# Kernel tuning notes

Hardware: AMD Instinct MI355X
Metric: run time of the kernel (lower is better)

Reference implementation:

```python
import jax, jax.numpy as jnp
import numpy as np

RADIUS = 3
T_STEPS = 2
NEG = -9.0e8
B, L, DEG = 256, 64, 6
FEAT, BOND, FP, OUT = 39, 10, 256, 1


def _leaky(x):
    return jax.nn.leaky_relu(x, 0.01)


def _gru(x, h, wih, whh, bih, bhh):
    # PyTorch GRUCell: gates ordered (r, z, n)
    gi = x @ wih.T + bih
    gh = h @ whh.T + bhh
    ir, iz, inn = jnp.split(gi, 3, axis=-1)
    hr, hz, hn = jnp.split(gh, 3, axis=-1)
    r = jax.nn.sigmoid(ir + hr)
    z = jax.nn.sigmoid(iz + hz)
    n = jnp.tanh(inn + r * hn)
    return (1.0 - z) * n + z * h


def _forward(atom_list, bond_list, atom_mask,
             atom_fc_w, atom_fc_b, neighbor_fc_w, neighbor_fc_b,
             align_w, align_b, attend_w, attend_b,
             gru_wih, gru_whh, gru_bih, gru_bhh,
             mol_align_w, mol_align_b, mol_attend_w, mol_attend_b,
             mol_gru_wih, mol_gru_whh, mol_gru_bih, mol_gru_bhh,
             out_w, out_b,
             atom_degree_list, bond_degree_list):
    b, l, _ = atom_list.shape
    mask = atom_mask[..., None]                                   # [B,L,1]
    atom_feature = _leaky(atom_list @ atom_fc_w.T + atom_fc_b)    # [B,L,FP]

    # per-molecule neighbor gather (padding index = L-1)
    bidx = jnp.arange(b)[:, None, None]
    atom_nb = atom_list[bidx, atom_degree_list]                    # [B,L,deg,FEAT]
    bond_nb = bond_list[bidx, bond_degree_list]                    # [B,L,deg,BOND]
    neighbor_feature = _leaky(
        jnp.concatenate([atom_nb, bond_nb], axis=-1) @ neighbor_fc_w.T + neighbor_fc_b
    )                                                              # [B,L,deg,FP]

    attend_mask = (atom_degree_list != l - 1).astype(atom_feature.dtype)[..., None]
    softmax_mask = jnp.where(atom_degree_list == l - 1, NEG, 0.0).astype(atom_feature.dtype)[..., None]

    for d in range(RADIUS):
        af_exp = jnp.broadcast_to(atom_feature[:, :, None, :], neighbor_feature.shape)
        feature_align = jnp.concatenate([af_exp, neighbor_feature], axis=-1)  # [B,L,deg,2FP]
        align_score = _leaky(feature_align @ align_w[d].T + align_b[d]) + softmax_mask
        attention_weight = jax.nn.softmax(align_score, axis=-2) * attend_mask
        attended = neighbor_feature @ attend_w[d].T + attend_b[d]
        context = jax.nn.elu(jnp.sum(attention_weight * attended, axis=-2))   # [B,L,FP]
        atom_feature = _gru(context.reshape(b * l, -1), atom_feature.reshape(b * l, -1),
                            gru_wih[d], gru_whh[d], gru_bih[d], gru_bhh[d]).reshape(b, l, -1)
        # faithful to original: self-feature broadcast across neighbor dim
        neighbor_feature = jnp.broadcast_to(jax.nn.relu(atom_feature)[:, :, None, :],
                                            neighbor_feature.shape)

    mol_feature = jnp.sum(jax.nn.relu(atom_feature) * mask, axis=-2)          # [B,FP]
    mol_softmax_mask = jnp.where(atom_mask == 0, NEG, 0.0).astype(atom_feature.dtype)[..., None]

    for _ in range(T_STEPS):
        m_exp = jnp.broadcast_to(mol_feature[:, None, :], atom_feature.shape)
        mol_align = jnp.concatenate([m_exp, atom_feature], axis=-1)           # [B,L,2FP]
        mol_score = _leaky(mol_align @ mol_align_w.T + mol_align_b) + mol_softmax_mask
        mol_w = jax.nn.softmax(mol_score, axis=-2) * mask
        attended = atom_feature @ mol_attend_w.T + mol_attend_b
        mol_context = jax.nn.elu(jnp.sum(mol_w * attended, axis=-2))
        mol_feature = _gru(mol_context, mol_feature,
                           mol_gru_wih, mol_gru_whh, mol_gru_bih, mol_gru_bhh)

    mol_prediction = mol_feature @ out_w.T + out_b
    return atom_feature, mol_prediction


def setup_inputs() -> dict:
    key = jax.random.key(0)
    ks = jax.random.split(key, 20)
    s = 0.05
    return {
        "atom_list": jax.random.normal(ks[0], (B, L, FEAT), jnp.float32),
        "bond_list": jax.random.normal(ks[1], (B, L, BOND), jnp.float32),
        "atom_degree_list": jax.random.randint(ks[2], (B, L, DEG), 0, L),
        "bond_degree_list": jax.random.randint(ks[3], (B, L, DEG), 0, L),
        "atom_mask": jnp.ones((B, L), jnp.float32),
        "atom_fc_w": jax.random.normal(ks[4], (FP, FEAT)) * s,
        "atom_fc_b": jnp.zeros((FP,)),
        "neighbor_fc_w": jax.random.normal(ks[5], (FP, FEAT + BOND)) * s,
        "neighbor_fc_b": jnp.zeros((FP,)),
        "align_w": jax.random.normal(ks[6], (RADIUS, 1, 2 * FP)) * s,
        "align_b": jnp.zeros((RADIUS, 1)),
        "attend_w": jax.random.normal(ks[7], (RADIUS, FP, FP)) * s,
        "attend_b": jnp.zeros((RADIUS, FP)),
        "gru_wih": jax.random.normal(ks[8], (RADIUS, 3 * FP, FP)) * s,
        "gru_whh": jax.random.normal(ks[9], (RADIUS, 3 * FP, FP)) * s,
        "gru_bih": jnp.zeros((RADIUS, 3 * FP)),
        "gru_bhh": jnp.zeros((RADIUS, 3 * FP)),
        "mol_align_w": jax.random.normal(ks[10], (1, 2 * FP)) * s,
        "mol_align_b": jnp.zeros((1,)),
        "mol_attend_w": jax.random.normal(ks[11], (FP, FP)) * s,
        "mol_attend_b": jnp.zeros((FP,)),
        "mol_gru_wih": jax.random.normal(ks[12], (3 * FP, FP)) * s,
        "mol_gru_whh": jax.random.normal(ks[13], (3 * FP, FP)) * s,
        "mol_gru_bih": jnp.zeros((3 * FP,)),
        "mol_gru_bhh": jnp.zeros((3 * FP,)),
        "out_w": jax.random.normal(ks[14], (OUT, FP)) * s,
        "out_b": jnp.zeros((OUT,)),
    }


def reference(atom_list, bond_list, atom_degree_list, bond_degree_list, atom_mask,
              atom_fc_w, atom_fc_b, neighbor_fc_w, neighbor_fc_b,
              align_w, align_b, attend_w, attend_b,
              gru_wih, gru_whh, gru_bih, gru_bhh,
              mol_align_w, mol_align_b, mol_attend_w, mol_attend_b,
              mol_gru_wih, mol_gru_whh, mol_gru_bih, mol_gru_bhh,
              out_w, out_b):
    return _forward(atom_list, bond_list, atom_mask,
                    atom_fc_w, atom_fc_b, neighbor_fc_w, neighbor_fc_b,
                    align_w, align_b, attend_w, attend_b,
                    gru_wih, gru_whh, gru_bih, gru_bhh,
                    mol_align_w, mol_align_b, mol_attend_w, mol_attend_b,
                    mol_gru_wih, mol_gru_whh, mol_gru_bih, mol_gru_bhh,
                    out_w, out_b,
                    atom_degree_list, bond_degree_list)
```

## Files before the change

### kernel.cpp

```cpp
#include <hip/hip_runtime.h>
#include <hip/hip_bf16.h>

#define NB 256
#define NL 64
#define DEG 6
#define FEAT 39
#define BOND 10
#define FP 256
#define NEGV (-9.0e8f)

using s16x8 = __attribute__((ext_vector_type(8))) short;
using f32x4 = __attribute__((ext_vector_type(4))) float;

__device__ __forceinline__ unsigned short f2bf(float f){
  unsigned u = __float_as_uint(f);
  u += 0x7fffu + ((u >> 16) & 1u);
  return (unsigned short)(u >> 16);
}
__device__ __forceinline__ float lo16(unsigned u){ return __uint_as_float(u << 16); }
__device__ __forceinline__ float hi16(unsigned u){ return __uint_as_float(u & 0xffff0000u); }

__device__ __forceinline__ float block_sum256(float v, float* scr){
  #pragma unroll
  for(int o=32;o>0;o>>=1) v += __shfl_down(v, o, 64);
  __syncthreads();
  if((threadIdx.x & 63) == 0) scr[threadIdx.x >> 6] = v;
  __syncthreads();
  return scr[0] + scr[1] + scr[2] + scr[3];
}
__device__ __forceinline__ float wave_allsum(float v){
  #pragma unroll
  for(int o=1;o<64;o<<=1) v += __shfl_xor(v, o, 64);
  return v;
}

#define CVT_N0 196608
#define CVT_N1 589824
#define CVT_N2 589824
#define CVT_N3 65536
#define CVT_N4 196608
#define CVT_N5 196608
#define CVT_TOT (CVT_N0+CVT_N1+CVT_N2+CVT_N3+CVT_N4+CVT_N5)

__global__ void k_cvt_all(const float* __restrict__ a0, const float* __restrict__ a1,
                          const float* __restrict__ a2, const float* __restrict__ a3,
                          const float* __restrict__ a4, const float* __restrict__ a5,
                          unsigned short* __restrict__ dst){
  int i = blockIdx.x*256 + threadIdx.x;
  int off = i; const float* src;
  if(off < CVT_N0) src = a0;
  else { off -= CVT_N0;
    if(off < CVT_N1) src = a1;
    else { off -= CVT_N1;
      if(off < CVT_N2) src = a2;
      else { off -= CVT_N2;
        if(off < CVT_N3) src = a3;
        else { off -= CVT_N3;
          if(off < CVT_N4) src = a4;
          else { off -= CVT_N4; src = a5; } } } } }
  dst[i] = f2bf(src[off]);
}

__global__ void k_tr(const float* __restrict__ aw, const float* __restrict__ nw,
                     float* __restrict__ afcT, unsigned short* __restrict__ nfcT){
  int i = blockIdx.x*256 + threadIdx.x;
  if(i < 40*256){
    int k = i >> 8, r = i & 255;
    afcT[i] = (k < FEAT) ? aw[r*FEAT + k] : 0.f;
  } else {
    int j = i - 40*256;
    int k = j >> 8, r = j & 255;
    nfcT[j] = (k < FEAT+BOND) ? f2bf(nw[r*(FEAT+BOND) + k]) : (unsigned short)0;
  }
}

__global__ __launch_bounds__(256) void k_atom4(const float* __restrict__ atom,
    const float* __restrict__ afcT, const float* __restrict__ bias, float* __restrict__ af){
  __shared__ float WT[40*256];
  __shared__ float x_s[4][40];
  const int t = threadIdx.x, bl0 = blockIdx.x*4;
  for(int v=t; v<2560; v+=256) *(float4*)&WT[v*4] = *(const float4*)&afcT[v*4];
  for(int idx=t; idx<4*FEAT; idx+=256){ int a=idx/FEAT, k=idx%FEAT; x_s[a][k]=atom[(bl0+a)*FEAT+k]; }
  if(t < 4) x_s[t][39] = 0.f;
  __syncthreads();
  const int w = t>>6, t0 = (t&63)*4, row = bl0 + w;
  float4 b4 = *(const float4*)&bias[t0];
  float acc[4] = {b4.x, b4.y, b4.z, b4.w};
  for(int k=0;k<40;++k){
    float iv = x_s[w][k];
    float4 wv = *(const float4*)&WT[(k<<8)+t0];
    acc[0]=fmaf(iv,wv.x,acc[0]); acc[1]=fmaf(iv,wv.y,acc[1]);
    acc[2]=fmaf(iv,wv.z,acc[2]); acc[3]=fmaf(iv,wv.w,acc[3]);
  }
  float4 o;
  o.x = acc[0]>0.f?acc[0]:0.01f*acc[0]; o.y = acc[1]>0.f?acc[1]:0.01f*acc[1];
  o.z = acc[2]>0.f?acc[2]:0.01f*acc[2]; o.w = acc[3]>0.f?acc[3]:0.01f*acc[3];
  *(float4*)&af[(size_t)row*FP + t0] = o;
}

__global__ __launch_bounds__(256) void k_nbr4(const float* __restrict__ atom,
    const float* __restrict__ bond, const int* __restrict__ adl, const int* __restrict__ bdl,
    const unsigned short* __restrict__ nfcT, const float* __restrict__ bn,
    const float* __restrict__ alw, const float* __restrict__ alb,
    const float* __restrict__ af, float* __restrict__ wnf, float* __restrict__ swb){
  __shared__ unsigned short WnT[52*256];
  __shared__ float in_s[4][DEG][52];
  __shared__ int   ai_s[4][DEG];
  const int t = threadIdx.x, bl0 = blockIdx.x*4;
  if(t < 24){ int a=t/6, d=t%6; ai_s[a][d] = adl[(bl0+a)*DEG + d]; }
  for(int v=t; v<1664; v+=256) *(s16x8*)&WnT[v*8] = *(const s16x8*)&nfcT[v*8];
  __syncthreads();
  for(int idx=t; idx<4*DEG*(FEAT+BOND); idx+=256){
    int a = idx/(DEG*(FEAT+BOND)), rem = idx%(DEG*(FEAT+BOND));
    int d = rem/(FEAT+BOND), k = rem%(FEAT+BOND);
    int bb = (bl0+a) >> 6;
    float v;
    if(k < FEAT) v = atom[((size_t)bb*NL + ai_s[a][d])*FEAT + k];
    else { int bi = bdl[(bl0+a)*DEG + d]; v = bond[((size_t)bb*NL + bi)*BOND + (k-FEAT)]; }
    in_s[a][d][k] = v;
  }
  if(t < 24){ int a=t/6, d=t%6; in_s[a][d][49]=0.f; in_s[a][d][50]=0.f; in_s[a][d][51]=0.f; }
  __syncthreads();
  const int w = t>>6, lane = t&63, t0 = lane*4, row = bl0 + w;
  float acc[DEG][4] = {};
  for(int k=0;k<52;++k){
    uint2 u = *(const uint2*)&WnT[(k<<8) + t0];
    float w0=lo16(u.x), w1=hi16(u.x), w2=lo16(u.y), w3=hi16(u.y);
    #pragma unroll
    for(int d=0;d<DEG;++d){
      float iv = in_s[w][d][k];
      acc[d][0]=fmaf(iv,w0,acc[d][0]); acc[d][1]=fmaf(iv,w1,acc[d][1]);
      acc[d][2]=fmaf(iv,w2,acc[d][2]); acc[d][3]=fmaf(iv,w3,acc[d][3]);
    }
  }
  float4 bnv = *(const float4*)&bn[t0];
  float bna[4] = {bnv.x, bnv.y, bnv.z, bnv.w};
  float nf[DEG][4];
  #pragma unroll
  for(int d=0;d<DEG;++d)
    #pragma unroll
    for(int j=0;j<4;++j){ float v = acc[d][j] + bna[j]; nf[d][j] = v>0.f ? v : 0.01f*v; }
  float4 af4 = *(const float4*)&af[(size_t)row*FP + t0];
  float4 a1  = *(const float4*)&alw[t0];
  float4 a2  = *(const float4*)&alw[FP + t0];
  float sa = wave_allsum(af4.x*a1.x + af4.y*a1.y + af4.z*a1.z + af4.w*a1.w);
  float sd[DEG];
  #pragma unroll
  for(int d=0;d<DEG;++d)
    sd[d] = wave_allsum(nf[d][0]*a2.x + nf[d][1]*a2.y + nf[d][2]*a2.z + nf[d][3]*a2.w);
  float ab = alb[0];
  float sc[DEG], msk[DEG];
  #pragma unroll
  for(int d=0;d<DEG;++d){
    float v = sa + sd[d] + ab;
    v = v>0.f ? v : 0.01f*v;
    msk[d] = (ai_s[w][d] == NL-1) ? 0.f : 1.f;
    sc[d] = v + (msk[d] > 0.f ? 0.f : NEGV);
  }
  float m = sc[0];
  #pragma unroll
  for(int d=1;d<DEG;++d) m = fmaxf(m, sc[d]);
  float e[DEG], Z = 0.f;
  #pragma unroll
  for(int d=0;d<DEG;++d){ e[d] = expf(sc[d]-m); Z += e[d]; }
  float wgt[DEG], sw = 0.f;
  #pragma unroll
  for(int d=0;d<DEG;++d){ wgt[d] = e[d]/Z*msk[d]; sw += wgt[d]; }
  float o[4] = {};
  #pragma unroll
  for(int d=0;d<DEG;++d)
    #pragma unroll
    for(int j=0;j<4;++j) o[j] = fmaf(wgt[d], nf[d][j], o[j]);
  float4 ov; ov.x=o[0]; ov.y=o[1]; ov.z=o[2]; ov.w=o[3];
  *(float4*)&wnf[(size_t)row*FP + t0] = ov;
  if(lane == 0) swb[row] = sw;
}

template<int MODE>
__global__ __launch_bounds__(256) void k_ctx_gemm(
    const float* __restrict__ Xsrc, const float* __restrict__ swb,
    const unsigned short* __restrict__ Wbf, const float* __restrict__ bat,
    unsigned short* __restrict__ ctxbf){
  __shared__ unsigned short A_lds[64][264];
  __shared__ unsigned short B_lds[64][264];
  const int t = threadIdx.x;
  const int m0 = (blockIdx.x >> 2) * 64, n0 = (blockIdx.x & 3) * 64;
  const int rb = t >> 4, cb = (t & 15) * 16;
  for(int i=0;i<4;++i){
    int row = i*16 + rb;
    const float* src = Xsrc + (size_t)(m0+row)*FP + cb;
    float mult = MODE ? swb[m0+row] : 1.f;
    unsigned short tmp[16];
    #pragma unroll
    for(int q=0;q<4;++q){
      float4 v = ((const float4*)src)[q];
      if(MODE){ v.x=fmaxf(v.x,0.f)*mult; v.y=fmaxf(v.y,0.f)*mult;
                v.z=fmaxf(v.z,0.f)*mult; v.w=fmaxf(v.w,0.f)*mult; }
      tmp[q*4+0]=f2bf(v.x); tmp[q*4+1]=f2bf(v.y); tmp[q*4+2]=f2bf(v.z); tmp[q*4+3]=f2bf(v.w);
    }
    *(s16x8*)&A_lds[row][cb]   = *(s16x8*)&tmp[0];
    *(s16x8*)&A_lds[row][cb+8] = *(s16x8*)&tmp[8];
    const unsigned short* wsrc = Wbf + (size_t)(n0+row)*FP + cb;
    *(s16x8*)&B_lds[row][cb]   = *(const s16x8*)&wsrc[0];
    *(s16x8*)&B_lds[row][cb+8] = *(const s16x8*)&wsrc[8];
  }
  __syncthreads();
  const int w = t>>6, lane = t&63, lr = lane&15, ks = lane>>4;
  const int wr = (w>>1)*32, wc = (w&1)*32;
  f32x4 acc[2][2] = {};
  #pragma unroll
  for(int kk=0;kk<8;++kk){
    int ko = kk*32 + ks*8;
    s16x8 a0 = *(const s16x8*)&A_lds[wr+lr][ko];
    s16x8 a1 = *(const s16x8*)&A_lds[wr+16+lr][ko];
    s16x8 b0 = *(const s16x8*)&B_lds[wc+lr][ko];
    s16x8 b1 = *(const s16x8*)&B_lds[wc+16+lr][ko];
    acc[0][0] = __builtin_amdgcn_mfma_f32_16x16x32_bf16(a0,b0,acc[0][0],0,0,0);
    acc[0][1] = __builtin_amdgcn_mfma_f32_16x16x32_bf16(a0,b1,acc[0][1],0,0,0);
    acc[1][0] = __builtin_amdgcn_mfma_f32_16x16x32_bf16(a1,b0,acc[1][0],0,0,0);
    acc[1][1] = __builtin_amdgcn_mfma_f32_16x16x32_bf16(a1,b1,acc[1][1],0,0,0);
  }
  #pragma unroll
  for(int fm=0;fm<2;++fm)
    #pragma unroll
    for(int fn=0;fn<2;++fn){
      int n = n0 + wc + fn*16 + lr;
      float batv = bat[n];
      #pragma unroll
      for(int j=0;j<4;++j){
        int m = m0 + wr + fm*16 + ks*4 + j;
        float v = acc[fm][fn][j] + swb[m]*batv;
        v = v > 0.f ? v : expm1f(v);
        ctxbf[(size_t)m*FP + n] = f2bf(v);
      }
    }
}

__global__ __launch_bounds__(256) void k_gates_gru(
    const unsigned short* __restrict__ ctxbf, const float* __restrict__ h_glob,
    const unsigned short* __restrict__ wihbf, const unsigned short* __restrict__ whhbf,
    const float* __restrict__ bih, const float* __restrict__ bhh,
    float* __restrict__ h_out){
  __shared__ unsigned short A_ctx[32][40];
  __shared__ unsigned short A_h[32][40];
  __shared__ unsigned short B_lds[6][64][40];
  const int t = threadIdx.x;
  const int m0 = (blockIdx.x >> 2) * 32, nc = (blockIdx.x & 3) * 64;
  const int w = t>>6, lane = t&63, lr = lane&15, ks = lane>>4;
  const int mh = (w>>1)*16, nh = (w&1)*32;
  f32x4 acc[6][2] = {};
  for(int kk=0;kk<8;++kk){
    const int k0 = kk*32;
    __syncthreads();
    {
      int row = t>>3, c4 = (t&7)*4;
      *(uint2*)&A_ctx[row][c4] = *(const uint2*)(ctxbf + (size_t)(m0+row)*FP + k0 + c4);
      float4 hv = *(const float4*)(h_glob + (size_t)(m0+row)*FP + k0 + c4);
      unsigned short ht[4] = {f2bf(hv.x), f2bf(hv.y), f2bf(hv.z), f2bf(hv.w)};
      *(uint2*)&A_h[row][c4] = *(uint2*)ht;
    }
    #pragma unroll
    for(int i=0;i<6;++i){
      int idx = i*256 + t;
      int s = idx >> 8, rem = idx & 255;
      int row = rem >> 2, c8 = (rem & 3)*8;
      const unsigned short* wsrc = (s < 3)
          ? wihbf + (size_t)(s*FP + nc + row)*FP + k0 + c8
          : whhbf + (size_t)((s-3)*FP + nc + row)*FP + k0 + c8;
      *(s16x8*)&B_lds[s][row][c8] = *(const s16x8*)wsrc;
    }
    __syncthreads();
    s16x8 ac = *(const s16x8*)&A_ctx[mh+lr][ks*8];
    s16x8 ah = *(const s16x8*)&A_h[mh+lr][ks*8];
    #pragma unroll
    for(int s=0;s<6;++s){
      s16x8 a = (s < 3) ? ac : ah;
      #pragma unroll
      for(int fn=0;fn<2;++fn){
        s16x8 b = *(const s16x8*)&B_lds[s][nh+fn*16+lr][ks*8];
        acc[s][fn] = __builtin_amdgcn_mfma_f32_16x16x32_bf16(a,b,acc[s][fn],0,0,0);
      }
    }
  }
  #pragma unroll
  for(int fn=0;fn<2;++fn){
    int n = nc + nh + fn*16 + lr;
    float bir = bih[n], biz = bih[FP+n], bin_ = bih[2*FP+n];
    float bhr = bhh[n], bhz = bhh[FP+n], bhn  = bhh[2*FP+n];
    #pragma unroll
    for(int j=0;j<4;++j){
      int m = m0 + mh + ks*4 + j;
      float h = h_glob[(size_t)m*FP + n];
      float ir = acc[0][fn][j]+bir, iz = acc[1][fn][j]+biz, inn = acc[2][fn][j]+bin_;
      float hr = acc[3][fn][j]+bhr, hz = acc[4][fn][j]+bhz, hn  = acc[5][fn][j]+bhn;
      float r = 1.f/(1.f + expf(-(ir+hr)));
      float z = 1.f/(1.f + expf(-(iz+hz)));
      float ng = tanhf(inn + r*hn);
      h_out[(size_t)m*FP + n] = (1.f-z)*ng + z*h;
    }
  }
}

__global__ __launch_bounds__(256) void k_lin_gemm(
    const float* __restrict__ Xsrc, const unsigned short* __restrict__ Wbf,
    const float* __restrict__ bias, float* __restrict__ Y){
  __shared__ unsigned short A_lds[64][264];
  __shared__ unsigned short B_lds[64][264];
  const int t = threadIdx.x;
  const int m0 = (blockIdx.x >> 2) * 64, n0 = (blockIdx.x & 3) * 64;
  const int rb = t >> 4, cb = (t & 15) * 16;
  for(int i=0;i<4;++i){
    int row = i*16 + rb;
    const float* src = Xsrc + (size_t)(m0+row)*FP + cb;
    unsigned short tmp[16];
    #pragma unroll
    for(int q=0;q<4;++q){
      float4 v = ((const float4*)src)[q];
      tmp[q*4+0]=f2bf(v.x); tmp[q*4+1]=f2bf(v.y); tmp[q*4+2]=f2bf(v.z); tmp[q*4+3]=f2bf(v.w);
    }
    *(s16x8*)&A_lds[row][cb]   = *(s16x8*)&tmp[0];
    *(s16x8*)&A_lds[row][cb+8] = *(s16x8*)&tmp[8];
    const unsigned short* wsrc = Wbf + (size_t)(n0+row)*FP + cb;
    *(s16x8*)&B_lds[row][cb]   = *(const s16x8*)&wsrc[0];
    *(s16x8*)&B_lds[row][cb+8] = *(const s16x8*)&wsrc[8];
  }
  __syncthreads();
  const int w = t>>6, lane = t&63, lr = lane&15, ks = lane>>4;
  const int wr = (w>>1)*32, wc = (w&1)*32;
  f32x4 acc[2][2] = {};
  #pragma unroll
  for(int kk=0;kk<8;++kk){
    int ko = kk*32 + ks*8;
    s16x8 a0 = *(const s16x8*)&A_lds[wr+lr][ko];
    s16x8 a1 = *(const s16x8*)&A_lds[wr+16+lr][ko];
    s16x8 b0 = *(const s16x8*)&B_lds[wc+lr][ko];
    s16x8 b1 = *(const s16x8*)&B_lds[wc+16+lr][ko];
    acc[0][0] = __builtin_amdgcn_mfma_f32_16x16x32_bf16(a0,b0,acc[0][0],0,0,0);
    acc[0][1] = __builtin_amdgcn_mfma_f32_16x16x32_bf16(a0,b1,acc[0][1],0,0,0);
    acc[1][0] = __builtin_amdgcn_mfma_f32_16x16x32_bf16(a1,b0,acc[1][0],0,0,0);
    acc[1][1] = __builtin_amdgcn_mfma_f32_16x16x32_bf16(a1,b1,acc[1][1],0,0,0);
  }
  #pragma unroll
  for(int fm=0;fm<2;++fm)
    #pragma unroll
    for(int fn=0;fn<2;++fn){
      int n = n0 + wc + fn*16 + lr;
      float bv = bias[n];
      #pragma unroll
      for(int j=0;j<4;++j){
        int m = m0 + wr + fm*16 + ks*4 + j;
        Y[(size_t)m*FP + n] = acc[fm][fn][j] + bv;
      }
    }
}

__global__ void k_finalize(const float* __restrict__ af, const float* __restrict__ mask,
                           float* __restrict__ molfeat, float* __restrict__ out_af){
  const int b = blockIdx.x, t = threadIdx.x;
  __shared__ float msk_s[NL];
  if(t < NL) msk_s[t] = mask[b*NL + t];
  __syncthreads();
  float mf = 0.f;
  for(int l=0;l<NL;++l){
    float v = af[(size_t)(b*NL + l)*FP + t];
    out_af[(size_t)(b*NL + l)*FP + t] = v;
    mf = fmaf(fmaxf(v,0.f), msk_s[l], mf);
  }
  molfeat[b*FP + t] = mf;
}

__global__ void k_mol_ctx(const float* __restrict__ af, const float* __restrict__ att,
    const float* __restrict__ mfin, const float* __restrict__ maw,
    const float* __restrict__ mabp, const float* __restrict__ mask,
    unsigned short* __restrict__ ctxb){
  const int b = blockIdx.x, t = threadIdx.x;
  __shared__ float mf_s[FP];
  __shared__ float sc_s[NL], aw_s[NL], scr[4];
  mf_s[t] = mfin[b*FP + t];
  __syncthreads();
  float sa = block_sum256(maw[t]*mf_s[t], scr);
  int l = t >> 2, q = t & 3;
  float p = 0.f;
  {
    const float* ar = af + (size_t)(b*NL + l)*FP + q*64;
    const float* w2 = maw + FP + q*64;
    for(int k=0;k<64;++k) p = fmaf(ar[k], w2[k], p);
  }
  p += __shfl_xor(p, 1, 64);
  p += __shfl_xor(p, 2, 64);
  if(q == 0){
    float mv = mask[b*NL + l];
    float v = sa + p + mabp[0];
    v = v > 0.f ? v : 0.01f*v;
    sc_s[l] = v + (mv == 0.f ? NEGV : 0.f);
  }
  __syncthreads();
  if(t < NL){
    float s = sc_s[t];
    float m = s;
    #pragma unroll
    for(int o=32;o>0;o>>=1) m = fmaxf(m, __shfl_xor(m, o, 64));
    float e = expf(s - m);
    float Z = e;
    #pragma unroll
    for(int o=32;o>0;o>>=1) Z += __shfl_xor(Z, o, 64);
    aw_s[t] = e / Z * mask[b*NL + t];
  }
  __syncthreads();
  float acc = 0.f;
  for(int l2=0;l2<NL;++l2) acc = fmaf(aw_s[l2], att[(size_t)(b*NL + l2)*FP + t], acc);
  float c = acc > 0.f ? acc : expm1f(acc);
  ctxb[b*FP + t] = f2bf(c);
}

__global__ void k_out(const float* __restrict__ molfeat, const float* __restrict__ ow,
                      const float* __restrict__ ob, float* __restrict__ outp){
  const int b = blockIdx.x, t = threadIdx.x;
  __shared__ float scr[4];
  float s = block_sum256(molfeat[b*FP + t]*ow[t], scr);
  if(t == 0) outp[b] = s + ob[0];
}

__global__ void k_atom_fc(const float* __restrict__ atom, const float* __restrict__ W,
                          const float* __restrict__ bias, float* __restrict__ af){
  const int row = blockIdx.x;
  const int t = threadIdx.x;
  __shared__ float x[FEAT];
  if(t < FEAT) x[t] = atom[row*FEAT + t];
  __syncthreads();
  float acc = bias[t];
  const float* wr = W + t*FEAT;
  #pragma unroll
  for(int k=0;k<FEAT;++k) acc = fmaf(x[k], wr[k], acc);
  af[row*FP + t] = acc > 0.f ? acc : 0.01f*acc;
}

__global__ void k_nbr_align(const float* __restrict__ atom, const float* __restrict__ bond,
    const int* __restrict__ adl, const int* __restrict__ bdl,
    const float* __restrict__ Wn, const float* __restrict__ bn,
    const float* __restrict__ alw, const float* __restrict__ alb,
    const float* __restrict__ af, float* __restrict__ wnf, float* __restrict__ swb){
  const int bl = blockIdx.x;
  const int b  = bl >> 6;
  const int t  = threadIdx.x;
  __shared__ float in_s[DEG][FEAT+BOND];
  __shared__ float nf_s[DEG][FP];
  __shared__ float af_s[FP];
  __shared__ int   ai[DEG];
  __shared__ float msk[DEG];
  __shared__ float sc[DEG];
  __shared__ float scr[4];
  if(t < DEG){ int a = adl[bl*DEG + t]; ai[t] = a; msk[t] = (a == NL-1) ? 0.f : 1.f; }
  af_s[t] = af[bl*FP + t];
  __syncthreads();
  for(int idx = t; idx < DEG*(FEAT+BOND); idx += FP){
    int d = idx / (FEAT+BOND), k = idx % (FEAT+BOND);
    float v;
    if(k < FEAT) v = atom[(b*NL + ai[d])*FEAT + k];
    else { int bi = bdl[bl*DEG + d]; v = bond[(b*NL + bi)*BOND + (k-FEAT)]; }
    in_s[d][k] = v;
  }
  __syncthreads();
  float acc[DEG];
  #pragma unroll
  for(int d=0;d<DEG;++d) acc[d] = 0.f;
  const float* wr = Wn + t*(FEAT+BOND);
  for(int k=0;k<FEAT+BOND;++k){
    float w = wr[k];
    #pragma unroll
    for(int d=0;d<DEG;++d) acc[d] = fmaf(in_s[d][k], w, acc[d]);
  }
  float bv = bn[t];
  #pragma unroll
  for(int d=0;d<DEG;++d){
    float v = acc[d] + bv;
    nf_s[d][t] = v > 0.f ? v : 0.01f*v;
  }
  __syncthreads();
  float aw1 = alw[t], aw2 = alw[FP + t];
  float sa = block_sum256(aw1*af_s[t], scr);
  float ab = alb[0];
  for(int d=0;d<DEG;++d){
    float s = block_sum256(aw2*nf_s[d][t], scr);
    if(t==0){
      float v = sa + s + ab;
      v = v > 0.f ? v : 0.01f*v;
      sc[d] = v + (msk[d] > 0.f ? 0.f : NEGV);
    }
  }
  __syncthreads();
  float m = sc[0];
  #pragma unroll
  for(int d=1;d<DEG;++d) m = fmaxf(m, sc[d]);
  float e[DEG], Z = 0.f;
  #pragma unroll
  for(int d=0;d<DEG;++d){ e[d] = expf(sc[d]-m); Z += e[d]; }
  float w_[DEG], sw = 0.f;
  #pragma unroll
  for(int d=0;d<DEG;++d){ w_[d] = e[d]/Z*msk[d]; sw += w_[d]; }
  float o = 0.f;
  #pragma unroll
  for(int d=0;d<DEG;++d) o = fmaf(w_[d], nf_s[d][t], o);
  wnf[bl*FP + t] = o;
  if(t==0) swb[bl] = sw;
}

template<int RELUX>
__global__ __launch_bounds__(256) void k_ctx_gru(
    const float* __restrict__ xsrc, const float* __restrict__ swb, float* __restrict__ af,
    const float* __restrict__ Wat, const float* __restrict__ bat,
    const float* __restrict__ wih, const float* __restrict__ whh,
    const float* __restrict__ bih, const float* __restrict__ bhh){
  const int R = 16;
  const int row0 = blockIdx.x * R;
  const int t = threadIdx.x;
  __shared__ __align__(16) float x_s[R][FP];
  __shared__ __align__(16) float h_s[R][FP];
  __shared__ float swb_s[R];
  if(t < R) swb_s[t] = swb[row0 + t];
  __syncthreads();
  #pragma unroll
  for(int r=0;r<R;++r){
    float h = af[(size_t)(row0+r)*FP + t];
    h_s[r][t] = h;
    if(RELUX) x_s[r][t] = fmaxf(h, 0.f) * swb_s[r];
    else      x_s[r][t] = xsrc[(size_t)(row0+r)*FP + t];
  }
  __syncthreads();
  float acc[R];
  #pragma unroll
  for(int r=0;r<R;++r) acc[r] = 0.f;
  const float4* wr = (const float4*)(Wat + (size_t)t*FP);
  for(int k4=0;k4<FP/4;++k4){
    float4 w = wr[k4];
    #pragma unroll
    for(int r=0;r<R;++r){
      float4 xv = ((const float4*)x_s[r])[k4];
      acc[r] = fmaf(xv.x,w.x,acc[r]); acc[r] = fmaf(xv.y,w.y,acc[r]);
      acc[r] = fmaf(xv.z,w.z,acc[r]); acc[r] = fmaf(xv.w,w.w,acc[r]);
// ... 62 lines not shown
    float zg = 1.f/(1.f + expf(-(iz+hz)));
    float ng = tanhf(inn + rg*hn);
    af[(size_t)(row0+r)*FP + t] = (1.f-zg)*ng + zg*h_s[r][t];
  }
}

__global__ void k_mol_att(const float* __restrict__ af, const float* __restrict__ maw,
    const float* __restrict__ mab, const float* __restrict__ mask,
    float* __restrict__ att, float* __restrict__ molfeat, float* __restrict__ out_af){
  const int b = blockIdx.x, t = threadIdx.x;
  __shared__ __align__(16) float a_s[32][FP];
  __shared__ float msk_s[NL];
  if(t < NL) msk_s[t] = mask[b*NL + t];
  __syncthreads();
  float mf = 0.f;
  const float4* wr = (const float4*)(maw + (size_t)t*FP);
  float mabv = mab[t];
  for(int half=0; half<2; ++half){
    #pragma unroll
    for(int i=0;i<32;++i){
      int l = half*32 + i;
      float v = af[(size_t)(b*NL + l)*FP + t];
      a_s[i][t] = v;
      out_af[(size_t)(b*NL + l)*FP + t] = v;
      mf = fmaf(fmaxf(v,0.f), msk_s[l], mf);
    }
    __syncthreads();
    float acc[32];
    #pragma unroll
    for(int i=0;i<32;++i) acc[i] = 0.f;
    for(int k4=0;k4<FP/4;++k4){
      float4 w = wr[k4];
      #pragma unroll
      for(int i=0;i<32;++i){
        float4 xv = ((const float4*)a_s[i])[k4];
        acc[i] = fmaf(xv.x,w.x,acc[i]); acc[i] = fmaf(xv.y,w.y,acc[i]);
        acc[i] = fmaf(xv.z,w.z,acc[i]); acc[i] = fmaf(xv.w,w.w,acc[i]);
      }
    }
    #pragma unroll
    for(int i=0;i<32;++i) att[(size_t)(b*NL + half*32 + i)*FP + t] = acc[i] + mabv;
    __syncthreads();
  }
  molfeat[b*FP + t] = mf;
}

__global__ void k_mol_step(const float* __restrict__ af, const float* __restrict__ att,
    float* __restrict__ molfeat, const float* __restrict__ maw, const float* __restrict__ mabp,
    const float* __restrict__ mask,
    const float* __restrict__ wih, const float* __restrict__ whh,
    const float* __restrict__ bih, const float* __restrict__ bhh){
  const int b = blockIdx.x, t = threadIdx.x;
  __shared__ __align__(16) float mf_s[FP];
  __shared__ __align__(16) float ctx_s[FP];
  __shared__ float sc_s[NL], aw_s[NL], scr[4];
  mf_s[t] = molfeat[b*FP + t];
  __syncthreads();
  float sa = block_sum256(maw[t]*mf_s[t], scr);
  int l = t >> 2, q = t & 3;
  float p = 0.f;
  {
    const float* ar = af + (size_t)(b*NL + l)*FP + q*64;
    const float* w2 = maw + FP + q*64;
    for(int k=0;k<64;++k) p = fmaf(ar[k], w2[k], p);
  }
  p += __shfl_xor(p, 1, 64);
  p += __shfl_xor(p, 2, 64);
  if(q == 0){
    float mv = mask[b*NL + l];
    float v = sa + p + mabp[0];
    v = v > 0.f ? v : 0.01f*v;
    sc_s[l] = v + (mv == 0.f ? NEGV : 0.f);
  }
  __syncthreads();
  if(t < NL){
    float s = sc_s[t];
    float m = s;
    #pragma unroll
    for(int o=32;o>0;o>>=1) m = fmaxf(m, __shfl_xor(m, o, 64));
    float e = expf(s - m);
    float Z = e;
    #pragma unroll
    for(int o=32;o>0;o>>=1) Z += __shfl_xor(Z, o, 64);
    aw_s[t] = e / Z * mask[b*NL + t];
  }
  __syncthreads();
  float acc = 0.f;
  for(int l2=0;l2<NL;++l2) acc = fmaf(aw_s[l2], att[(size_t)(b*NL + l2)*FP + t], acc);
  ctx_s[t] = acc > 0.f ? acc : expm1f(acc);
  __syncthreads();
  float air=0.f, aiz=0.f, ain=0.f, ahr=0.f, ahz=0.f, ahn=0.f;
  const float4* wirp=(const float4*)(wih + (size_t)t*FP);
  const float4* wizp=(const float4*)(wih + (size_t)(FP+t)*FP);
  const float4* winp=(const float4*)(wih + (size_t)(2*FP+t)*FP);
  const float4* whrp=(const float4*)(whh + (size_t)t*FP);
  const float4* whzp=(const float4*)(whh + (size_t)(FP+t)*FP);
  const float4* whnp=(const float4*)(whh + (size_t)(2*FP+t)*FP);
  for(int k4=0;k4<FP/4;++k4){
    float4 xv = ((const float4*)ctx_s)[k4];
    float4 hv = ((const float4*)mf_s)[k4];
    float4 f0=wirp[k4], f1=wizp[k4], f2=winp[k4];
    float4 g0=whrp[k4], g1=whzp[k4], g2=whnp[k4];
    air=fmaf(xv.x,f0.x,air); air=fmaf(xv.y,f0.y,air); air=fmaf(xv.z,f0.z,air); air=fmaf(xv.w,f0.w,air);
    aiz=fmaf(xv.x,f1.x,aiz); aiz=fmaf(xv.y,f1.y,aiz); aiz=fmaf(xv.z,f1.z,aiz); aiz=fmaf(xv.w,f1.w,aiz);
    ain=fmaf(xv.x,f2.x,ain); ain=fmaf(xv.y,f2.y,ain); ain=fmaf(xv.z,f2.z,ain); ain=fmaf(xv.w,f2.w,ain);
    ahr=fmaf(hv.x,g0.x,ahr); ahr=fmaf(hv.y,g0.y,ahr); ahr=fmaf(hv.z,g0.z,ahr); ahr=fmaf(hv.w,g0.w,ahr);
    ahz=fmaf(hv.x,g1.x,ahz); ahz=fmaf(hv.y,g1.y,ahz); ahz=fmaf(hv.z,g1.z,ahz); ahz=fmaf(hv.w,g1.w,ahz);
    ahn=fmaf(hv.x,g2.x,ahn); ahn=fmaf(hv.y,g2.y,ahn); ahn=fmaf(hv.z,g2.z,ahn); ahn=fmaf(hv.w,g2.w,ahn);
  }
  float ir=air+bih[t], iz=aiz+bih[FP+t], inn=ain+bih[2*FP+t];
  float hr=ahr+bhh[t], hz=ahz+bhh[FP+t], hn=ahn+bhh[2*FP+t];
  float rg = 1.f/(1.f + expf(-(ir+hr)));
  float zg = 1.f/(1.f + expf(-(iz+hz)));
  float ng = tanhf(inn + rg*hn);
  molfeat[b*FP + t] = (1.f-zg)*ng + zg*mf_s[t];
}

extern "C" void kernel_launch(void* const* d_in, const int* in_sizes, int n_in,
                              void* d_out, int out_size, void* d_ws, size_t ws_size,
                              hipStream_t stream){
  const float* atom_list = (const float*)d_in[0];
  const float* bond_list = (const float*)d_in[1];
  const int*   adl       = (const int*)d_in[2];
  const int*   bdl       = (const int*)d_in[3];
  const float* amask     = (const float*)d_in[4];
  const float* afc_w     = (const float*)d_in[5];
  const float* afc_b     = (const float*)d_in[6];
  const float* nfc_w     = (const float*)d_in[7];
  const float* nfc_b     = (const float*)d_in[8];
  const float* align_w   = (const float*)d_in[9];
  const float* align_b   = (const float*)d_in[10];
  const float* attend_w  = (const float*)d_in[11];
  const float* attend_b  = (const float*)d_in[12];
  const float* gru_wih   = (const float*)d_in[13];
  const float* gru_whh   = (const float*)d_in[14];
  const float* gru_bih   = (const float*)d_in[15];
  const float* gru_bhh   = (const float*)d_in[16];
  const float* mol_align_w  = (const float*)d_in[17];
  const float* mol_align_b  = (const float*)d_in[18];
  const float* mol_attend_w = (const float*)d_in[19];
  const float* mol_attend_b = (const float*)d_in[20];
  const float* mg_wih    = (const float*)d_in[21];
  const float* mg_whh    = (const float*)d_in[22];
  const float* mg_bih    = (const float*)d_in[23];
  const float* mg_bhh    = (const float*)d_in[24];
  const float* out_w     = (const float*)d_in[25];
  const float* out_b     = (const float*)d_in[26];

  float* out_af   = (float*)d_out;
  float* out_pred = out_af + (size_t)NB*NL*FP;

  const size_t NROW = (size_t)NB*NL;
  const size_t F32_CNT = 3*NROW*FP + NROW + 2*(size_t)NB*FP + 40*256;
  const size_t BF16_CNT = NROW*FP + CVT_TOT + 52*256;
  const size_t NEED = F32_CNT*4 + BF16_CNT*2;

  if(ws_size >= NEED){
    float* af_a    = (float*)d_ws;
    float* af_b    = af_a + NROW*FP;
    float* wnf     = af_b + NROW*FP;
    float* swb     = wnf  + NROW*FP;
    float* mf_a    = swb  + NROW;
    float* mf_b    = mf_a + (size_t)NB*FP;
    float* afcT    = mf_b + (size_t)NB*FP;
    unsigned short* ctxbf   = (unsigned short*)(afcT + 40*256);
    unsigned short* attw_bf = ctxbf + NROW*FP;
    unsigned short* wih_bf  = attw_bf + CVT_N0;
    unsigned short* whh_bf  = wih_bf + CVT_N1;
    unsigned short* maw_bf  = whh_bf + CVT_N2;
    unsigned short* mgih_bf = maw_bf + CVT_N3;
    unsigned short* mghh_bf = mgih_bf + CVT_N4;
    unsigned short* nfcT_bf = mghh_bf + CVT_N5;

    k_cvt_all<<<CVT_TOT/256, 256, 0, stream>>>(attend_w, gru_wih, gru_whh,
                                               mol_attend_w, mg_wih, mg_whh, attw_bf);
    k_tr<<<(40*256 + 52*256)/256, 256, 0, stream>>>(afc_w, nfc_w, afcT, nfcT_bf);

    k_atom4<<<NB*NL/4, 256, 0, stream>>>(atom_list, afcT, afc_b, af_a);
    k_nbr4<<<NB*NL/4, 256, 0, stream>>>(atom_list, bond_list, adl, bdl,
                                        nfcT_bf, nfc_b, align_w, align_b, af_a, wnf, swb);
    float* h_cur = af_a;
    float* h_nxt = af_b;
    for(int d=0; d<3; ++d){
      const unsigned short* Wat = attw_bf + (size_t)d*FP*FP;
      const float* bat = attend_b + (size_t)d*FP;
      const unsigned short* wih = wih_bf + (size_t)d*3*FP*FP;
      const unsigned short* whh = whh_bf + (size_t)d*3*FP*FP;
      const float* bih = gru_bih + (size_t)d*3*FP;
      const float* bhh = gru_bhh + (size_t)d*3*FP;
      if(d == 0)
        k_ctx_gemm<0><<<(NB*NL/64)*4, 256, 0, stream>>>(wnf, swb, Wat, bat, ctxbf);
      else
        k_ctx_gemm<1><<<(NB*NL/64)*4, 256, 0, stream>>>(h_cur, swb, Wat, bat, ctxbf);
      k_gates_gru<<<(NB*NL/32)*4, 256, 0, stream>>>(ctxbf, h_cur, wih, whh, bih, bhh, h_nxt);
      float* tmp = h_cur; h_cur = h_nxt; h_nxt = tmp;
    }
    k_lin_gemm<<<(NB*NL/64)*4, 256, 0, stream>>>(h_cur, maw_bf, mol_attend_b, wnf);
    k_finalize<<<NB, 256, 0, stream>>>(h_cur, amask, mf_a, out_af);
    float* m_cur = mf_a; float* m_nxt = mf_b;
    for(int s=0; s<2; ++s){
      k_mol_ctx<<<NB, 256, 0, stream>>>(h_cur, wnf, m_cur, mol_align_w, mol_align_b,
                                        amask, ctxbf);
      k_gates_gru<<<(NB/32)*4, 256, 0, stream>>>(ctxbf, m_cur, mgih_bf, mghh_bf,
                                                 mg_bih, mg_bhh, m_nxt);
      float* tmp = m_cur; m_cur = m_nxt; m_nxt = tmp;
    }
    k_out<<<NB, 256, 0, stream>>>(m_cur, out_w, out_b, out_pred);
  } else {
    float* af      = (float*)d_ws;
    float* wnf     = af  + NROW*FP;
    float* swb     = wnf + NROW*FP;
    float* molfeat = swb + NROW;

    k_atom_fc<<<NB*NL, FP, 0, stream>>>(atom_list, afc_w, afc_b, af);
    k_nbr_align<<<NB*NL, FP, 0, stream>>>(atom_list, bond_list, adl, bdl,
                                          nfc_w, nfc_b, align_w, align_b, af, wnf, swb);
    for(int d=0; d<3; ++d){
      const float* Wat = attend_w + (size_t)d*FP*FP;
      const float* bat = attend_b + (size_t)d*FP;
      const float* wih = gru_wih + (size_t)d*3*FP*FP;
      const float* whh = gru_whh + (size_t)d*3*FP*FP;
      const float* bih = gru_bih + (size_t)d*3*FP;
      const float* bhh = gru_bhh + (size_t)d*3*FP;
      if(d == 0) k_ctx_gru<0><<<NB*NL/16, FP, 0, stream>>>(wnf, swb, af, Wat, bat, wih, whh, bih, bhh);
      else       k_ctx_gru<1><<<NB*NL/16, FP, 0, stream>>>(af,  swb, af, Wat, bat, wih, whh, bih, bhh);
    }
    k_mol_att<<<NB, FP, 0, stream>>>(af, mol_attend_w, mol_attend_b, amask, wnf, molfeat, out_af);
    for(int s=0; s<2; ++s)
      k_mol_step<<<NB, FP, 0, stream>>>(af, wnf, molfeat, mol_align_w, mol_align_b, amask,
                                        mg_wih, mg_whh, mg_bih, mg_bhh);
    k_out<<<NB, FP, 0, stream>>>(molfeat, out_w, out_b, out_pred);
  }
}
```

Measured before the change: 337.6 us.

## Move neighbor FC to MFMA, enlarge GRU gate tile, vectorize mol-ctx dot

The neighbor feature FC and attention kernel now runs on bf16 MFMA tiles covering 16 atoms (96 neighbor rows) per block instead of scalar FMAs over 4 atoms. Neighbor inputs and activations are rounded to bf16 in LDS before the weighted sum. The atom-level GRU gates kernel is templated to process 64 rows per block, which reuses the B weight tiles across more rows. The mol-ctx dot product is vectorized with float4 loads. Together these aim to cut scalar ALU work and weight reloads, at the cost of extra bf16 rounding and higher register/LDS pressure.

```diff
diff --git a/kernel.cpp b/kernel.cpp
--- a/kernel.cpp
+++ b/kernel.cpp
@@ -17,8 +17,9 @@
   u += 0x7fffu + ((u >> 16) & 1u);
   return (unsigned short)(u >> 16);
 }
-__device__ __forceinline__ float lo16(unsigned u){ return __uint_as_float(u << 16); }
-__device__ __forceinline__ float hi16(unsigned u){ return __uint_as_float(u & 0xffff0000u); }
+__device__ __forceinline__ float bf2f(unsigned short s){
+  return __uint_as_float(((unsigned)s) << 16);
+}
 
 __device__ __forceinline__ float block_sum256(float v, float* scr){
   #pragma unroll
@@ -27,11 +28,6 @@
   if((threadIdx.x & 63) == 0) scr[threadIdx.x >> 6] = v;
   __syncthreads();
   return scr[0] + scr[1] + scr[2] + scr[3];
-}
-__device__ __forceinline__ float wave_allsum(float v){
-  #pragma unroll
-  for(int o=1;o<64;o<<=1) v += __shfl_xor(v, o, 64);
-  return v;
 }
 
 #define CVT_N0 196608
@@ -62,15 +58,15 @@
 }
 
 __global__ void k_tr(const float* __restrict__ aw, const float* __restrict__ nw,
-                     float* __restrict__ afcT, unsigned short* __restrict__ nfcT){
+                     float* __restrict__ afcT, unsigned short* __restrict__ nfcN){
   int i = blockIdx.x*256 + threadIdx.x;
   if(i < 40*256){
     int k = i >> 8, r = i & 255;
     afcT[i] = (k < FEAT) ? aw[r*FEAT + k] : 0.f;
   } else {
     int j = i - 40*256;
-    int k = j >> 8, r = j & 255;
-    nfcT[j] = (k < FEAT+BOND) ? f2bf(nw[r*(FEAT+BOND) + k]) : (unsigned short)0;
+    int n = j >> 6, k = j & 63;
+    nfcN[j] = (k < FEAT+BOND) ? f2bf(nw[n*(FEAT+BOND) + k]) : (unsigned short)0;
   }
 }
 
@@ -98,82 +94,150 @@
   *(float4*)&af[(size_t)row*FP + t0] = o;
 }
 
-__global__ __launch_bounds__(256) void k_nbr4(const float* __restrict__ atom,
-    const float* __restrict__ bond, const int* __restrict__ adl, const int* __restrict__ bdl,
-    const unsigned short* __restrict__ nfcT, const float* __restrict__ bn,
+__global__ __launch_bounds__(256) void k_nbr_mfma(
+    const float* __restrict__ atom, const float* __restrict__ bond,
+    const int* __restrict__ adl, const int* __restrict__ bdl,
+    const unsigned short* __restrict__ nfcN, const float* __restrict__ bn,
     const float* __restrict__ alw, const float* __restrict__ alb,
     const float* __restrict__ af, float* __restrict__ wnf, float* __restrict__ swb){
-  __shared__ unsigned short WnT[52*256];
-  __shared__ float in_s[4][DEG][52];
-  __shared__ int   ai_s[4][DEG];
-  const int t = threadIdx.x, bl0 = blockIdx.x*4;
-  if(t < 24){ int a=t/6, d=t%6; ai_s[a][d] = adl[(bl0+a)*DEG + d]; }
-  for(int v=t; v<1664; v+=256) *(s16x8*)&WnT[v*8] = *(const s16x8*)&nfcT[v*8];
-  __syncthreads();
-  for(int idx=t; idx<4*DEG*(FEAT+BOND); idx+=256){
-    int a = idx/(DEG*(FEAT+BOND)), rem = idx%(DEG*(FEAT+BOND));
-    int d = rem/(FEAT+BOND), k = rem%(FEAT+BOND);
-    int bb = (bl0+a) >> 6;
-    float v;
-    if(k < FEAT) v = atom[((size_t)bb*NL + ai_s[a][d])*FEAT + k];
-    else { int bi = bdl[(bl0+a)*DEG + d]; v = bond[((size_t)bb*NL + bi)*BOND + (k-FEAT)]; }
-    in_s[a][d][k] = v;
-  }
-  if(t < 24){ int a=t/6, d=t%6; in_s[a][d][49]=0.f; in_s[a][d][50]=0.f; in_s[a][d][51]=0.f; }
-  __syncthreads();
-  const int w = t>>6, lane = t&63, t0 = lane*4, row = bl0 + w;
-  float acc[DEG][4] = {};
-  for(int k=0;k<52;++k){
-    uint2 u = *(const uint2*)&WnT[(k<<8) + t0];
-    float w0=lo16(u.x), w1=hi16(u.x), w2=lo16(u.y), w3=hi16(u.y);
-    #pragma unroll
-    for(int d=0;d<DEG;++d){
-      float iv = in_s[w][d][k];
-      acc[d][0]=fmaf(iv,w0,acc[d][0]); acc[d][1]=fmaf(iv,w1,acc[d][1]);
-      acc[d][2]=fmaf(iv,w2,acc[d][2]); acc[d][3]=fmaf(iv,w3,acc[d][3]);
-    }
-  }
-  float4 bnv = *(const float4*)&bn[t0];
-  float bna[4] = {bnv.x, bnv.y, bnv.z, bnv.w};
-  float nf[DEG][4];
-  #pragma unroll
-  for(int d=0;d<DEG;++d)
-    #pragma unroll
-    for(int j=0;j<4;++j){ float v = acc[d][j] + bna[j]; nf[d][j] = v>0.f ? v : 0.01f*v; }
-  float4 af4 = *(const float4*)&af[(size_t)row*FP + t0];
-  float4 a1  = *(const float4*)&alw[t0];
-  float4 a2  = *(const float4*)&alw[FP + t0];
-  float sa = wave_allsum(af4.x*a1.x + af4.y*a1.y + af4.z*a1.z + af4.w*a1.w);
-  float sd[DEG];
-  #pragma unroll
-  for(int d=0;d<DEG;++d)
-    sd[d] = wave_allsum(nf[d][0]*a2.x + nf[d][1]*a2.y + nf[d][2]*a2.z + nf[d][3]*a2.w);
-  float ab = alb[0];
-  float sc[DEG], msk[DEG];
-  #pragma unroll
-  for(int d=0;d<DEG;++d){
-    float v = sa + sd[d] + ab;
-    v = v>0.f ? v : 0.01f*v;
-    msk[d] = (ai_s[w][d] == NL-1) ? 0.f : 1.f;
-    sc[d] = v + (msk[d] > 0.f ? 0.f : NEGV);
-  }
-  float m = sc[0];
-  #pragma unroll
-  for(int d=1;d<DEG;++d) m = fmaxf(m, sc[d]);
-  float e[DEG], Z = 0.f;
-  #pragma unroll
-  for(int d=0;d<DEG;++d){ e[d] = expf(sc[d]-m); Z += e[d]; }
-  float wgt[DEG], sw = 0.f;
-  #pragma unroll
-  for(int d=0;d<DEG;++d){ wgt[d] = e[d]/Z*msk[d]; sw += wgt[d]; }
-  float o[4] = {};
-  #pragma unroll
-  for(int d=0;d<DEG;++d)
-    #pragma unroll
-    for(int j=0;j<4;++j) o[j] = fmaf(wgt[d], nf[d][j], o[j]);
-  float4 ov; ov.x=o[0]; ov.y=o[1]; ov.z=o[2]; ov.w=o[3];
-  *(float4*)&wnf[(size_t)row*FP + t0] = ov;
-  if(lane == 0) swb[row] = sw;
+  __shared__ __align__(16) unsigned short U[96*264];
+  __shared__ int   ai_s[16][6];
+  __shared__ float sd_scr[4][96];
+  __shared__ float wgt_s[16][6];
+  __shared__ float sa_s[16];
+  const int t = threadIdx.x;
+  const int ga0 = blockIdx.x * 16;
+  if(t < 96) ai_s[t/6][t%6] = adl[(size_t)(ga0 + t/6)*DEG + (t%6)];
+  {
+    const s16x8* src = (const s16x8*)(nfcN + t*64);
+    #pragma unroll
+    for(int q=0;q<8;++q) *(s16x8*)&U[6912 + t*72 + q*8] = src[q];
+  }
+  __syncthreads();
+  for(int idx = t; idx < 96*64; idx += 256){
+    int row = idx >> 6, k = idx & 63;
+    int a = row/6, d = row - a*6;
+    int ga = ga0 + a, b = ga >> 6;
+    float v = 0.f;
+    if(k < FEAT) v = atom[((size_t)b*NL + ai_s[a][d])*FEAT + k];
+    else if(k < FEAT+BOND){ int bi = bdl[(size_t)ga*DEG + d]; v = bond[((size_t)b*NL + bi)*BOND + (k-FEAT)]; }
+    U[row*72 + k] = f2bf(v);
+  }
+  const int w = t>>6, lane = t&63, lr = lane&15, ks = lane>>4;
+  {
+    int a = w*4 + ks, c0 = lr*16;
+    const float* ap = af + (size_t)(ga0+a)*FP + c0;
+    const float* wp = alw + c0;
+    float s = 0.f;
+    #pragma unroll
+    for(int k=0;k<16;++k) s = fmaf(ap[k], wp[k], s);
+    s += __shfl_xor(s, 1, 64); s += __shfl_xor(s, 2, 64);
+    s += __shfl_xor(s, 4, 64); s += __shfl_xor(s, 8, 64);
+    if(lr == 0) sa_s[a] = s;
+  }
+  __syncthreads();
+  const int n0w = w*64;
+  f32x4 acc[6][4] = {};
+  #pragma unroll
+  for(int kk=0;kk<2;++kk){
+    int ko = kk*32 + ks*8;
+    s16x8 bfr[4];
+    #pragma unroll
+    for(int nf=0;nf<4;++nf) bfr[nf] = *(const s16x8*)&U[6912 + (n0w + nf*16 + lr)*72 + ko];
+    #pragma unroll
+    for(int mf=0;mf<6;++mf){
+      s16x8 afr = *(const s16x8*)&U[(mf*16 + lr)*72 + ko];
+      #pragma unroll
+      for(int nf=0;nf<4;++nf)
+        acc[mf][nf] = __builtin_amdgcn_mfma_f32_16x16x32_bf16(afr, bfr[nf], acc[mf][nf], 0,0,0);
+    }
+  }
+  float bnv[4], a2v[4];
+  #pragma unroll
+  for(int nf=0;nf<4;++nf){ int col = n0w + nf*16 + lr; bnv[nf] = bn[col]; a2v[nf] = alw[FP + col]; }
+  float p[6][4];
+  #pragma unroll
+  for(int mf=0;mf<6;++mf){
+    #pragma unroll
+    for(int j=0;j<4;++j) p[mf][j] = 0.f;
+    #pragma unroll
+    for(int nf=0;nf<4;++nf){
+      #pragma unroll
+      for(int j=0;j<4;++j){
+        float v = acc[mf][nf][j] + bnv[nf];
+        v = v > 0.f ? v : 0.01f*v;
+        acc[mf][nf][j] = v;
+        p[mf][j] = fmaf(a2v[nf], v, p[mf][j]);
+      }
+    }
+  }
+  #pragma unroll
+  for(int mf=0;mf<6;++mf)
+    #pragma unroll
+    for(int j=0;j<4;++j){
+      float v = p[mf][j];
+      v += __shfl_xor(v, 1, 64); v += __shfl_xor(v, 2, 64);
+      v += __shfl_xor(v, 4, 64); v += __shfl_xor(v, 8, 64);
+      p[mf][j] = v;
+    }
+  __syncthreads();
+  if(lr == 0){
+    #pragma unroll
+    for(int mf=0;mf<6;++mf)
+      #pragma unroll
+      for(int j=0;j<4;++j) sd_scr[w][mf*16 + ks*4 + j] = p[mf][j];
+  }
+  #pragma unroll
+  for(int mf=0;mf<6;++mf)
+    #pragma unroll
+    for(int nf=0;nf<4;++nf)
+      #pragma unroll
+      for(int j=0;j<4;++j)
+        U[(mf*16 + ks*4 + j)*264 + (n0w + nf*16 + lr)] = f2bf(acc[mf][nf][j]);
+  __syncthreads();
+  if(t < 16){
+    int a = t, ga = ga0 + a;
+    float ab = alb[0];
+    float sc[6], msk[6];
+    #pragma unroll
+    for(int d=0;d<6;++d){
+      int r = a*6 + d;
+      float sd = sd_scr[0][r] + sd_scr[1][r] + sd_scr[2][r] + sd_scr[3][r];
+      float v = sa_s[a] + sd + ab;
+      v = v>0.f ? v : 0.01f*v;
+      msk[d] = (ai_s[a][d] == NL-1) ? 0.f : 1.f;
+      sc[d] = v + (msk[d] > 0.f ? 0.f : NEGV);
+    }
+    float m = sc[0];
+    #pragma unroll
+    for(int d=1;d<6;++d) m = fmaxf(m, sc[d]);
+    float e[6], Z = 0.f;
+    #pragma unroll
+    for(int d=0;d<6;++d){ e[d] = expf(sc[d]-m); Z += e[d]; }
+    float sw = 0.f;
+    #pragma unroll
+    for(int d=0;d<6;++d){ float wv = e[d]/Z*msk[d]; wgt_s[a][d] = wv; sw += wv; }
+    swb[ga] = sw;
+  }
+  __syncthreads();
+  {
+    int a = t >> 4, c0 = (t & 15) * 16;
+    float wgt[6];
+    #pragma unroll
+    for(int d=0;d<6;++d) wgt[d] = wgt_s[a][d];
+    float o[16];
+    #pragma unroll
+    for(int c=0;c<16;++c) o[c] = 0.f;
+    #pragma unroll
+    for(int d=0;d<6;++d){
+      int r = a*6 + d;
+      #pragma unroll
+      for(int c=0;c<16;++c) o[c] = fmaf(wgt[d], bf2f(U[r*264 + c0 + c]), o[c]);
+    }
+    float* dst = wnf + (size_t)(ga0+a)*FP + c0;
+    #pragma unroll
+    for(int c=0;c<16;++c) dst[c] = o[c];
+  }
 }
 
 template<int MODE>
@@ -236,24 +300,27 @@
     }
 }
 
+template<int MT>
 __global__ __launch_bounds__(256) void k_gates_gru(
     const unsigned short* __restrict__ ctxbf, const float* __restrict__ h_glob,
     const unsigned short* __restrict__ wihbf, const unsigned short* __restrict__ whhbf,
     const float* __restrict__ bih, const float* __restrict__ bhh,
     float* __restrict__ h_out){
-  __shared__ unsigned short A_ctx[32][40];
-  __shared__ unsigned short A_h[32][40];
+  constexpr int MFR = MT/32;
+  __shared__ unsigned short A_ctx[MT][40];
+  __shared__ unsigned short A_h[MT][40];
   __shared__ unsigned short B_lds[6][64][40];
   const int t = threadIdx.x;
-  const int m0 = (blockIdx.x >> 2) * 32, nc = (blockIdx.x & 3) * 64;
+  const int m0 = (blockIdx.x >> 2) * MT, nc = (blockIdx.x & 3) * 64;
   const int w = t>>6, lane = t&63, lr = lane&15, ks = lane>>4;
-  const int mh = (w>>1)*16, nh = (w&1)*32;
-  f32x4 acc[6][2] = {};
+  const int mh = (w>>1)*(MT/2), nh = (w&1)*32;
+  f32x4 acc[6][MFR][2] = {};
   for(int kk=0;kk<8;++kk){
     const int k0 = kk*32;
     __syncthreads();
-    {
-      int row = t>>3, c4 = (t&7)*4;
+    #pragma unroll
+    for(int rr=0; rr<MFR; ++rr){
+      int row = rr*32 + (t>>3), c4 = (t&7)*4;
       *(uint2*)&A_ctx[row][c4] = *(const uint2*)(ctxbf + (size_t)(m0+row)*FP + k0 + c4);
       float4 hv = *(const float4*)(h_glob + (size_t)(m0+row)*FP + k0 + c4);
       unsigned short ht[4] = {f2bf(hv.x), f2bf(hv.y), f2bf(hv.z), f2bf(hv.w)};
@@ -270,15 +337,22 @@
       *(s16x8*)&B_lds[s][row][c8] = *(const s16x8*)wsrc;
     }
     __syncthreads();
-    s16x8 ac = *(const s16x8*)&A_ctx[mh+lr][ks*8];
-    s16x8 ah = *(const s16x8*)&A_h[mh+lr][ks*8];
+    s16x8 ac[MFR], ah[MFR];
+    #pragma unroll
+    for(int mf=0;mf<MFR;++mf){
+      ac[mf] = *(const s16x8*)&A_ctx[mh + mf*16 + lr][ks*8];
+      ah[mf] = *(const s16x8*)&A_h[mh + mf*16 + lr][ks*8];
+    }
     #pragma unroll
     for(int s=0;s<6;++s){
-      s16x8 a = (s < 3) ? ac : ah;
-      #pragma unroll
-      for(int fn=0;fn<2;++fn){
-        s16x8 b = *(const s16x8*)&B_lds[s][nh+fn*16+lr][ks*8];
-        acc[s][fn] = __builtin_amdgcn_mfma_f32_16x16x32_bf16(a,b,acc[s][fn],0,0,0);
+      #pragma unroll
+      for(int mf=0;mf<MFR;++mf){
+        s16x8 a = (s < 3) ? ac[mf] : ah[mf];
+        #pragma unroll
+        for(int fn=0;fn<2;++fn){
+          s16x8 b = *(const s16x8*)&B_lds[s][nh+fn*16+lr][ks*8];
+          acc[s][mf][fn] = __builtin_amdgcn_mfma_f32_16x16x32_bf16(a,b,acc[s][mf][fn],0,0,0);
+        }
       }
     }
   }
@@ -288,15 +362,18 @@
     float bir = bih[n], biz = bih[FP+n], bin_ = bih[2*FP+n];
     float bhr = bhh[n], bhz = bhh[FP+n], bhn  = bhh[2*FP+n];
     #pragma unroll
-    for(int j=0;j<4;++j){
-      int m = m0 + mh + ks*4 + j;
-      float h = h_glob[(size_t)m*FP + n];
-      float ir = acc[0][fn][j]+bir, iz = acc[1][fn][j]+biz, inn = acc[2][fn][j]+bin_;
-      float hr = acc[3][fn][j]+bhr, hz = acc[4][fn][j]+bhz, hn  = acc[5][fn][j]+bhn;
-      float r = 1.f/(1.f + expf(-(ir+hr)));
-      float z = 1.f/(1.f + expf(-(iz+hz)));
-      float ng = tanhf(inn + r*hn);
-      h_out[(size_t)m*FP + n] = (1.f-z)*ng + z*h;
+    for(int mf=0;mf<MFR;++mf){
+      #pragma unroll
+      for(int j=0;j<4;++j){
+        int m = m0 + mh + mf*16 + ks*4 + j;
+        float h = h_glob[(size_t)m*FP + n];
+        float ir = acc[0][mf][fn][j]+bir, iz = acc[1][mf][fn][j]+biz, inn = acc[2][mf][fn][j]+bin_;
+        float hr = acc[3][mf][fn][j]+bhr, hz = acc[4][mf][fn][j]+bhz, hn  = acc[5][mf][fn][j]+bhn;
+        float r = 1.f/(1.f + expf(-(ir+hr)));
+        float z = 1.f/(1.f + expf(-(iz+hz)));
+        float ng = tanhf(inn + r*hn);
+        h_out[(size_t)m*FP + n] = (1.f-z)*ng + z*h;
+      }
     }
   }
 }
@@ -382,9 +459,14 @@
   int l = t >> 2, q = t & 3;
   float p = 0.f;
   {
-    const float* ar = af + (size_t)(b*NL + l)*FP + q*64;
-    const float* w2 = maw + FP + q*64;
-    for(int k=0;k<64;++k) p = fmaf(ar[k], w2[k], p);
+    const float4* ar = (const float4*)(af + (size_t)(b*NL + l)*FP + q*64);
+    const float4* w2 = (const float4*)(maw + FP + q*64);
+    #pragma unroll
+    for(int k=0;k<16;++k){
+      float4 a = ar[k], ww = w2[k];
+      p = fmaf(a.x,ww.x,p); p = fmaf(a.y,ww.y,p);
+      p = fmaf(a.z,ww.z,p); p = fmaf(a.w,ww.w,p);
+    }
   }
   p += __shfl_xor(p, 1, 64);
   p += __shfl_xor(p, 2, 64);
@@ -753,7 +835,7 @@
 
   const size_t NROW = (size_t)NB*NL;
   const size_t F32_CNT = 3*NROW*FP + NROW + 2*(size_t)NB*FP + 40*256;
-  const size_t BF16_CNT = NROW*FP + CVT_TOT + 52*256;
+  const size_t BF16_CNT = NROW*FP + CVT_TOT + 256*64;
   const size_t NEED = F32_CNT*4 + BF16_CNT*2;
 
   if(ws_size >= NEED){
@@ -771,15 +853,16 @@
     unsigned short* maw_bf  = whh_bf + CVT_N2;
     unsigned short* mgih_bf = maw_bf + CVT_N3;
     unsigned short* mghh_bf = mgih_bf + CVT_N4;
-    unsigned short* nfcT_bf = mghh_bf + CVT_N5;
+    unsigned short* nfcN_bf = mghh_bf + CVT_N5;
 
     k_cvt_all<<<CVT_TOT/256, 256, 0, stream>>>(attend_w, gru_wih, gru_whh,
                                                mol_attend_w, mg_wih, mg_whh, attw_bf);
-    k_tr<<<(40*256 + 52*256)/256, 256, 0, stream>>>(afc_w, nfc_w, afcT, nfcT_bf);
+    k_tr<<<(40*256 + 256*64)/256, 256, 0, stream>>>(afc_w, nfc_w, afcT, nfcN_bf);
 
     k_atom4<<<NB*NL/4, 256, 0, stream>>>(atom_list, afcT, afc_b, af_a);
-    k_nbr4<<<NB*NL/4, 256, 0, stream>>>(atom_list, bond_list, adl, bdl,
-                                        nfcT_bf, nfc_b, align_w, align_b, af_a, wnf, swb);
+    k_nbr_mfma<<<NB*NL/16, 256, 0, stream>>>(atom_list, bond_list, adl, bdl,
+                                             nfcN_bf, nfc_b, align_w, align_b,
+                                             af_a, wnf, swb);
     float* h_cur = af_a;
     float* h_nxt = af_b;
     for(int d=0; d<3; ++d){
@@ -793,7 +876,7 @@
         k_ctx_gemm<0><<<(NB*NL/64)*4, 256, 0, stream>>>(wnf, swb, Wat, bat, ctxbf);
       else
         k_ctx_gemm<1><<<(NB*NL/64)*4, 256, 0, stream>>>(h_cur, swb, Wat, bat, ctxbf);
-      k_gates_gru<<<(NB*NL/32)*4, 256, 0, stream>>>(ctxbf, h_cur, wih, whh, bih, bhh, h_nxt);
+      k_gates_gru<64><<<(NB*NL/64)*4, 256, 0, stream>>>(ctxbf, h_cur, wih, whh, bih, bhh, h_nxt);
       float* tmp = h_cur; h_cur = h_nxt; h_nxt = tmp;
     }
     k_lin_gemm<<<(NB*NL/64)*4, 256, 0, stream>>>(h_cur, maw_bf, mol_attend_b, wnf);
@@ -802,8 +885,8 @@
     for(int s=0; s<2; ++s){
       k_mol_ctx<<<NB, 256, 0, stream>>>(h_cur, wnf, m_cur, mol_align_w, mol_align_b,
                                         amask, ctxbf);
-      k_gates_gru<<<(NB/32)*4, 256, 0, stream>>>(ctxbf, m_cur, mgih_bf, mghh_bf,
-                                                 mg_bih, mg_bhh, m_nxt);
+      k_gates_gru<32><<<(NB/32)*4, 256, 0, stream>>>(ctxbf, m_cur, mgih_bf, mghh_bf,
+                                                     mg_bih, mg_bhh, m_nxt);
       float* tmp = m_cur; m_cur = m_nxt; m_nxt = tmp;
     }
     k_out<<<NB, 256, 0, stream>>>(m_cur, out_w, out_b, out_pred);
```

New measurement: 377.7 us. 11.9% more time.
